# Kernel optimization log

Measured on AMD Instinct MI355X. Metric: run time of the kernel, lower is better.

Reference implementation:

```python
import jax, jax.numpy as jnp
import numpy as np
import math

B, S, HID = 2, 2048, 2048
NH, NKV, HD = 16, 4, 128
N_REP = NH // NKV
THETA = 1000000.0


def apply_rope(x, position_ids, theta=THETA):
    # x: (B, H, S, D), position_ids: (B, S)
    d = x.shape[-1]
    freqs = 1.0 / (theta ** (jnp.arange(0, d, 2, dtype=jnp.float32) / d))  # (D/2,)
    angles = position_ids.astype(jnp.float32)[:, :, None] * freqs[None, None, :]  # (B,S,D/2)
    cos = jnp.cos(angles)[:, None, :, :]  # (B,1,S,D/2)
    sin = jnp.sin(angles)[:, None, :, :]
    x_even = x[..., 0::2]
    x_odd = x[..., 1::2]
    rot_even = x_even * cos - x_odd * sin
    rot_odd = x_even * sin + x_odd * cos
    out = jnp.stack([rot_even, rot_odd], axis=-1)  # (B,H,S,D/2,2)
    return out.reshape(x.shape)


def setup_inputs() -> dict:
    key = jax.random.key(0)
    ks = jax.random.split(key, 6)
    x = jax.random.normal(ks[0], (B, S, HID), dtype=jnp.float32)
    position_ids = jnp.broadcast_to(jnp.arange(S, dtype=jnp.int64)[None, :], (B, S))
    # causal additive mask: 0 on/below diagonal, large negative above
    causal = jnp.where(jnp.tril(jnp.ones((S, S), dtype=bool)), 0.0, -1e9).astype(jnp.float32)
    attention_mask = jnp.broadcast_to(causal[None, None, :, :], (B, 1, S, S))
    sc = 1.0 / math.sqrt(HID)
    Wq = jax.random.normal(ks[1], (HID, NH * HD), dtype=jnp.float32) * sc
    Wk = jax.random.normal(ks[2], (HID, NKV * HD), dtype=jnp.float32) * sc
    Wv = jax.random.normal(ks[3], (HID, NKV * HD), dtype=jnp.float32) * sc
    Wo = jax.random.normal(ks[4], (NH * HD, HID), dtype=jnp.float32) * sc
    return {"x": x, "position_ids": position_ids, "attention_mask": attention_mask,
            "Wq": Wq, "Wk": Wk, "Wv": Wv, "Wo": Wo}


def reference(x, position_ids, attention_mask, Wq, Wk, Wv, Wo):
    b, s, _ = x.shape
    q = (x @ Wq).reshape(b, s, NH, HD).transpose(0, 2, 1, 3)   # (B,NH,S,D)
    k = (x @ Wk).reshape(b, s, NKV, HD).transpose(0, 2, 1, 3)  # (B,NKV,S,D)
    v = (x @ Wv).reshape(b, s, NKV, HD).transpose(0, 2, 1, 3)
    q = apply_rope(q, position_ids)
    k = apply_rope(k, position_ids)
    # repeat_kv: expand KV heads to match Q heads
    k = jnp.repeat(k, N_REP, axis=1)  # (B,NH,S,D)
    v = jnp.repeat(v, N_REP, axis=1)
    scale = 1.0 / math.sqrt(HD)
    scores = jnp.einsum('bhqd,bhkd->bhqk', q, k) * scale
    scores = scores + attention_mask
    attn = jax.nn.softmax(scores, axis=-1)
    out = jnp.einsum('bhqk,bhkd->bhqd', attn, v)
    out = out.transpose(0, 2, 1, 3).reshape(b, s, NH * HD)
    return out @ Wo
```

## Files before the change

### kernel.cpp

```cpp
#include <hip/hip_runtime.h>
#include <hip/hip_bf16.h>

#define S_LEN 2048
#define HID_D 2048
#define NH 16
#define NKV 4
#define HD 128
#define BATCH 2

typedef __hip_bfloat16 bf16;
using f32x4 = __attribute__((ext_vector_type(4))) float;
using s16x8 = __attribute__((ext_vector_type(8))) short;

__device__ __forceinline__ f32x4 mfma_16x16x32(s16x8 a, s16x8 b, f32x4 c) {
  return __builtin_amdgcn_mfma_f32_16x16x32_bf16(a, b, c, 0, 0, 0);
}

__device__ __forceinline__ void gload16(const void* g, void* l) {
  __builtin_amdgcn_global_load_lds(
      (const __attribute__((address_space(1))) void*)g,
      (__attribute__((address_space(3))) void*)l, 16, 0, 0);
}

__device__ __forceinline__ unsigned int pk2bf(float a, float b) {
  __hip_bfloat16 lo = __float2bfloat16(a), hi = __float2bfloat16(b);
  return ((unsigned int)*(unsigned short*)&hi << 16) | *(unsigned short*)&lo;
}

__global__ __launch_bounds__(256) void convert_bf16_k(const float* __restrict__ in,
                                                      bf16* __restrict__ out) {
  int i = (blockIdx.x * 256 + threadIdx.x) * 4;
  float4 v = *(const float4*)&in[i];
  out[i + 0] = __float2bfloat16(v.x);
  out[i + 1] = __float2bfloat16(v.y);
  out[i + 2] = __float2bfloat16(v.z);
  out[i + 3] = __float2bfloat16(v.w);
}

__global__ __launch_bounds__(256) void transpose_convert_k(const float* __restrict__ in,
                                                           bf16* __restrict__ out,
                                                           int K, int N) {
  __shared__ float tile[32][33];
  int n0 = blockIdx.x * 32, k0 = blockIdx.y * 32;
  int tx = threadIdx.x, ty = threadIdx.y;
#pragma unroll
  for (int i = ty; i < 32; i += 8) tile[i][tx] = in[(size_t)(k0 + i) * N + n0 + tx];
  __syncthreads();
#pragma unroll
  for (int i = ty; i < 32; i += 8)
    out[(size_t)(n0 + i) * K + k0 + tx] = __float2bfloat16(tile[tx][i]);
}

__global__ __launch_bounds__(512) void gemm256_k(const bf16* __restrict__ A,
                                                 const bf16* __restrict__ Bt,
                                                 bf16* __restrict__ C,
                                                 int M, int N, int K) {
  __shared__ bf16 Asm[2][256 * 64];
  __shared__ bf16 Bsm[2][256 * 64];
  const int tid = threadIdx.x;
  const int lane = tid & 63, wid = tid >> 6;
  const int fr = lane & 15, hi = lane >> 4;

  const int bid = blockIdx.y * gridDim.x + blockIdx.x;
  const int nwg = gridDim.x * gridDim.y;
  const int swz = (bid & 7) * (nwg >> 3) + (bid >> 3);
  const int m0 = (swz % gridDim.x) * 256;
  const int n0 = (swz / gridDim.x) * 256;

  const bf16* Ag = A + (size_t)m0 * K;
  const bf16* Bg = Bt + (size_t)n0 * K;

  auto stageT = [&](const bf16* src, bf16* ldsBase, int k0) {
#pragma unroll
    for (int c = 0; c < 4; ++c) {
      int byte = tid * 16 + c * 8192;
      int row = byte >> 7;
      int col = byte & 127;
      int colSw = col ^ ((row & 7) << 4);
      gload16((const char*)(src + (size_t)row * K + k0) + colSw,
              (char*)ldsBase + byte);
    }
  };

  f32x4 acc[4][8];
#pragma unroll
  for (int m = 0; m < 4; ++m)
#pragma unroll
    for (int n = 0; n < 8; ++n) acc[m][n] = (f32x4){0.f, 0.f, 0.f, 0.f};

  const int r0 = (wid >> 1) * 64;
  const int c0 = (wid & 1) * 128;
  const int NT = K >> 6;

  stageT(Ag, &Asm[0][0], 0);
  stageT(Bg, &Bsm[0][0], 0);
  asm volatile("s_waitcnt vmcnt(0)" ::: "memory");
  __builtin_amdgcn_s_barrier();

  for (int t = 0; t < NT; ++t) {
    const int cur = t & 1;
    const int nxt = cur ^ 1;
    const int kn = (t + 1) << 6;
    const bool more = (t + 1) < NT;
#pragma unroll
    for (int p = 0; p < 2; ++p) {
      s16x8 af[4], bq[8];
#pragma unroll
      for (int m = 0; m < 4; ++m) {
        int r = r0 + m * 16 + fr;
        int cb = (p * 64 + hi * 16) ^ ((r & 7) << 4);
        af[m] = *(const s16x8*)((const char*)&Asm[cur][0] + r * 128 + cb);
      }
#pragma unroll
      for (int n = 0; n < 8; ++n) {
        int bn = c0 + n * 16 + fr;
        int cb = (p * 64 + hi * 16) ^ ((bn & 7) << 4);
        bq[n] = *(const s16x8*)((const char*)&Bsm[cur][0] + bn * 128 + cb);
      }
      if (p == 0) {
        if (more) {
          stageT(Ag, &Asm[nxt][0], kn);
          stageT(Bg, &Bsm[nxt][0], kn);
        }
      } else {
        asm volatile("s_waitcnt vmcnt(0)" ::: "memory");
      }
      __builtin_amdgcn_s_barrier();

      __builtin_amdgcn_s_setprio(1);
#pragma unroll
      for (int m = 0; m < 4; ++m)
#pragma unroll
        for (int n = 0; n < 8; ++n)
          acc[m][n] = mfma_16x16x32(af[m], bq[n], acc[m][n]);
      __builtin_amdgcn_s_setprio(0);
    }
  }

#pragma unroll
  for (int m = 0; m < 4; ++m)
#pragma unroll
    for (int n = 0; n < 8; ++n) {
      const int row = m0 + r0 + m * 16 + hi * 4;
      const int col = n0 + c0 + n * 16 + fr;
#pragma unroll
      for (int r = 0; r < 4; ++r)
        C[(size_t)(row + r) * N + col] = __float2bfloat16(acc[m][n][r]);
    }
}

__global__ __launch_bounds__(256) void gemm128sq_k(const bf16* __restrict__ A,
                                                   const bf16* __restrict__ Bt,
                                                   float* __restrict__ C,
                                                   int M, int N, int K) {
  __shared__ bf16 Asm[2][128 * 64];
  __shared__ bf16 Bsm[2][128 * 64];
  const int tid = threadIdx.x;
  const int lane = tid & 63, wid = tid >> 6;
  const int fr = lane & 15, hi = lane >> 4;

  const int bid = blockIdx.y * gridDim.x + blockIdx.x;
  const int nwg = gridDim.x * gridDim.y;
  const int swz = (bid & 7) * (nwg >> 3) + (bid >> 3);
  const int m0 = (swz % gridDim.x) * 128;
  const int n0 = (swz / gridDim.x) * 128;

  const bf16* Ag = A + (size_t)m0 * K;
  const bf16* Bg = Bt + (size_t)n0 * K;

  auto stageT = [&](const bf16* src, bf16* ldsBase, int k0) {
#pragma unroll
    for (int c = 0; c < 4; ++c) {
      int byte = tid * 16 + c * 4096;
      int row = byte >> 7;
      int col = byte & 127;
      int colSw = col ^ ((row & 7) << 4);
      gload16((const char*)(src + (size_t)row * K + k0) + colSw,
              (char*)ldsBase + byte);
    }
  };

  f32x4 acc[4][4];
#pragma unroll
  for (int m = 0; m < 4; ++m)
#pragma unroll
    for (int n = 0; n < 4; ++n) acc[m][n] = (f32x4){0.f, 0.f, 0.f, 0.f};

  const int r0 = (wid >> 1) * 64;
  const int c0 = (wid & 1) * 64;
  const int NT = K >> 6;

  stageT(Ag, &Asm[0][0], 0);
  stageT(Bg, &Bsm[0][0], 0);
  asm volatile("s_waitcnt vmcnt(0)" ::: "memory");
  __builtin_amdgcn_s_barrier();

  for (int t = 0; t < NT; ++t) {
    const int cur = t & 1;
    const int nxt = cur ^ 1;
    const int kn = (t + 1) << 6;
    const bool more = (t + 1) < NT;
#pragma unroll
    for (int p = 0; p < 2; ++p) {
      s16x8 af[4], bq[4];
#pragma unroll
      for (int m = 0; m < 4; ++m) {
        int r = r0 + m * 16 + fr;
        int cb = (p * 64 + hi * 16) ^ ((r & 7) << 4);
        af[m] = *(const s16x8*)((const char*)&Asm[cur][0] + r * 128 + cb);
      }
#pragma unroll
      for (int n = 0; n < 4; ++n) {
        int bn = c0 + n * 16 + fr;
        int cb = (p * 64 + hi * 16) ^ ((bn & 7) << 4);
        bq[n] = *(const s16x8*)((const char*)&Bsm[cur][0] + bn * 128 + cb);
      }
      if (p == 0) {
        if (more) {
          stageT(Ag, &Asm[nxt][0], kn);
          stageT(Bg, &Bsm[nxt][0], kn);
        }
      } else {
        asm volatile("s_waitcnt vmcnt(0)" ::: "memory");
      }
      __builtin_amdgcn_s_barrier();

      __builtin_amdgcn_s_setprio(1);
#pragma unroll
      for (int m = 0; m < 4; ++m)
#pragma unroll
        for (int n = 0; n < 4; ++n)
          acc[m][n] = mfma_16x16x32(af[m], bq[n], acc[m][n]);
      __builtin_amdgcn_s_setprio(0);
    }
  }

#pragma unroll
  for (int m = 0; m < 4; ++m)
#pragma unroll
    for (int n = 0; n < 4; ++n) {
      const int row = m0 + r0 + m * 16 + hi * 4;
      const int col = n0 + c0 + n * 16 + fr;
#pragma unroll
      for (int r = 0; r < 4; ++r)
        C[(size_t)(row + r) * N + col] = acc[m][n][r];
    }
}

__global__ __launch_bounds__(256) void rope_q_k(const bf16* __restrict__ qkv,
                                                const int* __restrict__ pos_ids,
                                                bf16* __restrict__ Q) {
  int idx = blockIdx.x * 256 + threadIdx.x;
  int i = idx & 63;
  int h = (idx >> 6) & 15;
  int s = (idx >> 10) & 2047;
  int b = idx >> 21;
  const float kscale = 0.12751841418861862f;
  float pos = (float)pos_ids[b * S_LEN + s];
  float freq = exp2f((float)i * -0.31143075889569023f);
  float ang = pos * freq;
  float sn, cs;
  sincosf(ang, &sn, &cs);
  const bf16* src = qkv + (size_t)(b * S_LEN + s) * 3072 + h * HD + 2 * i;
  float e = __bfloat162float(src[0]), o = __bfloat162float(src[1]);
  bf16* dst = Q + ((size_t)(b * NH + h) * S_LEN + s) * HD + 2 * i;
  dst[0] = __float2bfloat16((e * cs - o * sn) * kscale);
  dst[1] = __float2bfloat16((e * sn + o * cs) * kscale);
}

__global__ __launch_bounds__(256) void rope_k_k(const bf16* __restrict__ qkv,
                                                const int* __restrict__ pos_ids,
                                                bf16* __restrict__ Kd) {
  int idx = blockIdx.x * 256 + threadIdx.x;
  int i = idx & 63;
  int kvh = (idx >> 6) & 3;
  int s = (idx >> 8) & 2047;
  int b = idx >> 19;
  float pos = (float)pos_ids[b * S_LEN + s];
  float freq = exp2f((float)i * -0.31143075889569023f);
  float ang = pos * freq;
  float sn, cs;
  sincosf(ang, &sn, &cs);
  const bf16* src = qkv + (size_t)(b * S_LEN + s) * 3072 + 2048 + kvh * HD + 2 * i;
  float e = __bfloat162float(src[0]), o = __bfloat162float(src[1]);
  bf16* dst = Kd + ((size_t)(b * NKV + kvh) * S_LEN + s) * HD + 2 * i;
  dst[0] = __float2bfloat16(e * cs - o * sn);
  dst[1] = __float2bfloat16(e * sn + o * cs);
}

__global__ __launch_bounds__(256) void v_trans_k(const bf16* __restrict__ qkv,
                                                 bf16* __restrict__ Vt) {
  __shared__ unsigned short tile[32][33];
  const int tx = threadIdx.x, ty = threadIdx.y;
  const int s0 = blockIdx.x * 32;
  const int d0 = blockIdx.y * 32;
  const int b = blockIdx.z >> 2, kvh = blockIdx.z & 3;
  const unsigned short* src = (const unsigned short*)qkv + 2560 + kvh * HD;
#pragma unroll
  for (int i = ty; i < 32; i += 8)
    tile[i][tx] = src[(size_t)(b * S_LEN + s0 + i) * 3072 + d0 + tx];
  __syncthreads();
  unsigned short* dst = (unsigned short*)Vt + (size_t)(b * NKV + kvh) * HD * S_LEN;
#pragma unroll
  for (int i = ty; i < 32; i += 8)
    dst[(size_t)(d0 + i) * S_LEN + s0 + tx] = tile[tx][i];
}

__global__ __launch_bounds__(512) void attn_k(const bf16* __restrict__ Q,
                                              const bf16* __restrict__ K,
                                              const bf16* __restrict__ Vt,
                                              bf16* __restrict__ Aout) {
  __shared__ __align__(16) char KsB[2][8320];
  __shared__ __align__(16) char VsB[2][10240];
  __shared__ __align__(16) char PsB[8][2560];

  const int tid = threadIdx.x;
  const int lane = tid & 63, wid = tid >> 6;
  const int fr = lane & 15, hi = lane >> 4;
  const int pi = blockIdx.x, h = blockIdx.y, b = blockIdx.z;
  const int kvh = h >> 2;
  const bf16* Qh = Q + (size_t)(b * NH + h) * S_LEN * HD;
  const bf16* Kh = K + (size_t)(b * NKV + kvh) * S_LEN * HD;
  const bf16* Vh = Vt + (size_t)(b * NKV + kvh) * HD * S_LEN;

  const int qb = (wid < 4) ? pi : (15 - pi);
  const int q0w = qb * 128 + (wid & 3) * 32;
  const int nsteps = 4 * (15 - pi) + 4;

  s16x8 qf[2][4];
#pragma unroll
  for (int u = 0; u < 2; ++u)
#pragma unroll
    for (int ks = 0; ks < 4; ++ks)
      qf[u][ks] = *(const s16x8*)&Qh[(size_t)(q0w + u * 16 + fr) * HD + ks * 32 + hi * 8];

  f32x4 o[2][8];
#pragma unroll
  for (int u = 0; u < 2; ++u)
#pragma unroll
    for (int ds = 0; ds < 8; ++ds) o[u][ds] = (f32x4){0.f, 0.f, 0.f, 0.f};
  float lacc[2][4];
#pragma unroll
  for (int u = 0; u < 2; ++u)
#pragma unroll
    for (int r = 0; r < 4; ++r) lacc[u][r] = 0.f;

  auto stageK = [&](int bufi, int kv0) {
    gload16((const char*)Kh + ((size_t)(kv0 + wid * 4)) * 256 + lane * 16,
            &KsB[bufi][0] + wid * 1040);
  };
  const int vd = tid >> 2;
  const int vko = (tid & 3) * 8;
  auto vload = [&](int kv0) {
    return *(const s16x8*)&Vh[(size_t)vd * S_LEN + kv0 + vko];
  };

  stageK(0, 0);
  {
    s16x8 v0 = vload(0);
    *(s16x8*)(&VsB[0][0] + vd * 80 + (tid & 3) * 16) = v0;
  }
  __syncthreads();

  int buf = 0;
  for (int s = 0; s < nsteps; ++s) {
    const int kv0 = s * 32;
    const bool more = (s + 1) < nsteps;
    s16x8 vnext = {};
    if (more) {
      stageK(buf ^ 1, kv0 + 32);
      vnext = vload(kv0 + 32);
    }

    if (kv0 <= q0w) {
      const bool diag = (kv0 == q0w);
      f32x4 sg[2][2];
#pragma unroll
      for (int u = 0; u < 2; ++u)
#pragma unroll
        for (int kv = 0; kv < 2; ++kv) sg[u][kv] = (f32x4){0.f, 0.f, 0.f, 0.f};
#pragma unroll
      for (int kv = 0; kv < 2; ++kv) {
        const int row = 2 * fr + kv;
        const char* kbase = &KsB[buf][0] + (row >> 2) * 1040 + (row & 3) * 256;
#pragma unroll
        for (int ks = 0; ks < 4; ++ks) {
          s16x8 kf = *(const s16x8*)(kbase + ks * 64 + hi * 16);
          sg[0][kv] = mfma_16x16x32(qf[0][ks], kf, sg[0][kv]);
          sg[1][kv] = mfma_16x16x32(qf[1][ks], kf, sg[1][kv]);
        }
      }

#pragma unroll
      for (int u = 0; u < 2; ++u)
#pragma unroll
        for (int r = 0; r < 4; ++r) {
          float p0 = __builtin_exp2f(sg[u][0][r]);
          float p1 = __builtin_exp2f(sg[u][1][r]);
          if (diag) {
            const int qrow = u * 16 + hi * 4 + r;
            p0 = (2 * fr <= qrow) ? p0 : 0.f;
            p1 = (2 * fr + 1 <= qrow) ? p1 : 0.f;
          }
          lacc[u][r] += p0 + p1;
          const int prow = u * 16 + hi * 4 + r;
          *(unsigned int*)(&PsB[wid][0] + prow * 80 + fr * 4) = pk2bf(p0, p1);
        }
      __builtin_amdgcn_wave_barrier();

      s16x8 pf[2];
#pragma unroll
      for (int u = 0; u < 2; ++u)
        pf[u] = *(const s16x8*)(&PsB[wid][0] + (u * 16 + fr) * 80 + hi * 16);
      __builtin_amdgcn_wave_barrier();

#pragma unroll
      for (int ds = 0; ds < 8; ++ds) {
        s16x8 vf = *(const s16x8*)(&VsB[buf][0] + (ds * 16 + fr) * 80 + hi * 16);
        o[0][ds] = mfma_16x16x32(pf[0], vf, o[0][ds]);
        o[1][ds] = mfma_16x16x32(pf[1], vf, o[1][ds]);
      }
    }

    if (more)
      *(s16x8*)(&VsB[buf ^ 1][0] + vd * 80 + (tid & 3) * 16) = vnext;
    __syncthreads();
    buf ^= 1;
  }

#pragma unroll
  for (int u = 0; u < 2; ++u)
#pragma unroll
    for (int r = 0; r < 4; ++r) {
      float l = lacc[u][r];
      l += __shfl_xor(l, 1, 16);
      l += __shfl_xor(l, 2, 16);
      l += __shfl_xor(l, 4, 16);
      l += __shfl_xor(l, 8, 16);
      float inv = 1.0f / l;
      const int srow = q0w + u * 16 + hi * 4 + r;
      bf16* orow = Aout + ((size_t)b * S_LEN + srow) * HID_D + h * HD;
#pragma unroll
      for (int ds = 0; ds < 8; ++ds)
        orow[ds * 16 + fr] = __float2bfloat16(o[u][ds][r] * inv);
    }
}

extern "C" void kernel_launch(void* const* d_in, const int* in_sizes, int n_in,
                              void* d_out, int out_size, void* d_ws, size_t ws_size,
                              hipStream_t stream) {
  const float* x = (const float*)d_in[0];
  const int* pos = (const int*)d_in[1];
  const float* Wq = (const float*)d_in[3];
  const float* Wk = (const float*)d_in[4];
  const float* Wv = (const float*)d_in[5];
  const float* Wo = (const float*)d_in[6];
  float* out = (float*)d_out;

  char* ws = (char*)d_ws;
  size_t off = 0;
  auto alloc = [&](size_t bytes) {
    char* p = ws + off;
    off += (bytes + 255) & ~(size_t)255;
    return p;
  };
  bf16* xb = (bf16*)alloc((size_t)4096 * 2048 * 2);
  bf16* WqkvT = (bf16*)alloc((size_t)3072 * 2048 * 2);
  bf16* WoT = (bf16*)alloc((size_t)2048 * 2048 * 2);
  bf16* qkv = (bf16*)alloc((size_t)4096 * 3072 * 2);
  bf16* Qb = (bf16*)alloc((size_t)BATCH * NH * S_LEN * HD * 2);
  bf16* Kb = (bf16*)alloc((size_t)BATCH * NKV * S_LEN * HD * 2);
  bf16* Vtb = (bf16*)alloc((size_t)BATCH * NKV * HD * S_LEN * 2);
  bf16* aout = (bf16*)qkv;

  convert_bf16_k<<<8192, 256, 0, stream>>>(x, xb);
  dim3 tb(32, 8);
  transpose_convert_k<<<dim3(64, 64), tb, 0, stream>>>(Wq, WqkvT, 2048, 2048);
  transpose_convert_k<<<dim3(16, 64), tb, 0, stream>>>(Wk, WqkvT + (size_t)2048 * 2048, 2048, 512);
  transpose_convert_k<<<dim3(16, 64), tb, 0, stream>>>(Wv, WqkvT + (size_t)2560 * 2048, 2048, 512);
  transpose_convert_k<<<dim3(64, 64), tb, 0, stream>>>(Wo, WoT, 2048, 2048);

  gemm256_k<<<dim3(16, 12), 512, 0, stream>>>(xb, WqkvT, qkv, 4096, 3072, 2048);

  rope_q_k<<<16384, 256, 0, stream>>>(qkv, pos, Qb);
  rope_k_k<<<4096, 256, 0, stream>>>(qkv, pos, Kb);
  v_trans_k<<<dim3(64, 4, 8), tb, 0, stream>>>(qkv, Vtb);

  attn_k<<<dim3(8, NH, BATCH), 512, 0, stream>>>(Qb, Kb, Vtb, aout);

  gemm128sq_k<<<dim3(32, 16), 256, 0, stream>>>(aout, WoT, out, 4096, 2048, 2048);
}
```

Before: 233.9 us.

## Split attention into one q-block per workgroup with swizzled async K/V staging

Removes the paired-q-block load balancing (8 waves covering blocks pi and 15-pi). Each 256-thread workgroup now handles a single 128-row q block, launched heaviest-first, over a 16-wide grid. K and V tiles are both staged with direct global-to-LDS loads using an XOR swizzle instead of padding, and the register round-trip for V is dropped. This gives more, smaller workgroups and less LDS per block, at the cost of uneven per-block work that relies on the reversed launch order for balance.

```diff
diff --git a/kernel.cpp b/kernel.cpp
--- a/kernel.cpp
+++ b/kernel.cpp
@@ -306,26 +306,48 @@
     dst[(size_t)(d0 + i) * S_LEN + s0 + tx] = tile[tx][i];
 }
 
-__global__ __launch_bounds__(512) void attn_k(const bf16* __restrict__ Q,
+__global__ __launch_bounds__(256) void attn_k(const bf16* __restrict__ Q,
                                               const bf16* __restrict__ K,
                                               const bf16* __restrict__ Vt,
                                               bf16* __restrict__ Aout) {
-  __shared__ __align__(16) char KsB[2][8320];
-  __shared__ __align__(16) char VsB[2][10240];
-  __shared__ __align__(16) char PsB[8][2560];
+  __shared__ __align__(16) char KsB[2][8192];
+  __shared__ __align__(16) char VsB[2][8192];
+  __shared__ __align__(16) char PsB[4][2560];
 
   const int tid = threadIdx.x;
   const int lane = tid & 63, wid = tid >> 6;
   const int fr = lane & 15, hi = lane >> 4;
-  const int pi = blockIdx.x, h = blockIdx.y, b = blockIdx.z;
+  const int qb = 15 - blockIdx.x;
+  const int h = blockIdx.y, b = blockIdx.z;
   const int kvh = h >> 2;
   const bf16* Qh = Q + (size_t)(b * NH + h) * S_LEN * HD;
   const bf16* Kh = K + (size_t)(b * NKV + kvh) * S_LEN * HD;
   const bf16* Vh = Vt + (size_t)(b * NKV + kvh) * HD * S_LEN;
 
-  const int qb = (wid < 4) ? pi : (15 - pi);
-  const int q0w = qb * 128 + (wid & 3) * 32;
-  const int nsteps = 4 * (15 - pi) + 4;
+  const int q0w = qb * 128 + wid * 32;
+  const int nsteps = 4 * qb + 4;
+
+  auto stageK = [&](int bufi, int kv0) {
+#pragma unroll
+    for (int c = 0; c < 2; ++c) {
+      int X = tid * 16 + c * 4096;
+      int row = X >> 8, col = X & 255;
+      int colSw = col ^ (((row >> 1) & 7) << 4);
+      gload16((const char*)Kh + (size_t)(kv0 + row) * 256 + colSw,
+              &KsB[bufi][0] + X);
+    }
+  };
+  auto stageV = [&](int bufi, int kv0) {
+#pragma unroll
+    for (int c = 0; c < 2; ++c) {
+      int X = tid * 16 + c * 4096;
+      int line = X >> 7, off = X & 127;
+      int offS = off ^ ((line & 7) << 4);
+      int d = 2 * line + (offS >> 6);
+      gload16((const char*)Vh + (size_t)d * (S_LEN * 2) + (size_t)kv0 * 2 + (offS & 63),
+              &VsB[bufi][0] + X);
+    }
+  };
 
   s16x8 qf[2][4];
 #pragma unroll
@@ -345,31 +367,16 @@
 #pragma unroll
     for (int r = 0; r < 4; ++r) lacc[u][r] = 0.f;
 
-  auto stageK = [&](int bufi, int kv0) {
-    gload16((const char*)Kh + ((size_t)(kv0 + wid * 4)) * 256 + lane * 16,
-            &KsB[bufi][0] + wid * 1040);
-  };
-  const int vd = tid >> 2;
-  const int vko = (tid & 3) * 8;
-  auto vload = [&](int kv0) {
-    return *(const s16x8*)&Vh[(size_t)vd * S_LEN + kv0 + vko];
-  };
-
   stageK(0, 0);
-  {
-    s16x8 v0 = vload(0);
-    *(s16x8*)(&VsB[0][0] + vd * 80 + (tid & 3) * 16) = v0;
-  }
+  stageV(0, 0);
   __syncthreads();
 
   int buf = 0;
   for (int s = 0; s < nsteps; ++s) {
     const int kv0 = s * 32;
-    const bool more = (s + 1) < nsteps;
-    s16x8 vnext = {};
-    if (more) {
+    if (s + 1 < nsteps) {
       stageK(buf ^ 1, kv0 + 32);
-      vnext = vload(kv0 + 32);
+      stageV(buf ^ 1, kv0 + 32);
     }
 
     if (kv0 <= q0w) {
@@ -378,16 +385,17 @@
 #pragma unroll
       for (int u = 0; u < 2; ++u)
 #pragma unroll
-        for (int kv = 0; kv < 2; ++kv) sg[u][kv] = (f32x4){0.f, 0.f, 0.f, 0.f};
-#pragma unroll
-      for (int kv = 0; kv < 2; ++kv) {
-        const int row = 2 * fr + kv;
-        const char* kbase = &KsB[buf][0] + (row >> 2) * 1040 + (row & 3) * 256;
+        for (int kvi = 0; kvi < 2; ++kvi) sg[u][kvi] = (f32x4){0.f, 0.f, 0.f, 0.f};
+#pragma unroll
+      for (int kvi = 0; kvi < 2; ++kvi) {
+        const int row = 2 * fr + kvi;
+        const char* kb_ = &KsB[buf][0] + row * 256;
+        const int sw = ((row >> 1) & 7) << 4;
 #pragma unroll
         for (int ks = 0; ks < 4; ++ks) {
-          s16x8 kf = *(const s16x8*)(kbase + ks * 64 + hi * 16);
-          sg[0][kv] = mfma_16x16x32(qf[0][ks], kf, sg[0][kv]);
-          sg[1][kv] = mfma_16x16x32(qf[1][ks], kf, sg[1][kv]);
+          s16x8 kf = *(const s16x8*)(kb_ + ((ks * 64 + hi * 16) ^ sw));
+          sg[0][kvi] = mfma_16x16x32(qf[0][ks], kf, sg[0][kvi]);
+          sg[1][kvi] = mfma_16x16x32(qf[1][ks], kf, sg[1][kvi]);
         }
       }
 
@@ -398,9 +406,9 @@
           float p0 = __builtin_exp2f(sg[u][0][r]);
           float p1 = __builtin_exp2f(sg[u][1][r]);
           if (diag) {
-            const int qrow = u * 16 + hi * 4 + r;
-            p0 = (2 * fr <= qrow) ? p0 : 0.f;
-            p1 = (2 * fr + 1 <= qrow) ? p1 : 0.f;
+            const int rowrel = u * 16 + hi * 4 + r;
+            p0 = (2 * fr <= rowrel) ? p0 : 0.f;
+            p1 = (2 * fr + 1 <= rowrel) ? p1 : 0.f;
           }
           lacc[u][r] += p0 + p1;
           const int prow = u * 16 + hi * 4 + r;
@@ -416,14 +424,15 @@
 
 #pragma unroll
       for (int ds = 0; ds < 8; ++ds) {
-        s16x8 vf = *(const s16x8*)(&VsB[buf][0] + (ds * 16 + fr) * 80 + hi * 16);
+        const int d = ds * 16 + fr;
+        const int line = d >> 1;
+        const int off = ((d & 1) * 64 + hi * 16) ^ ((line & 7) << 4);
+        s16x8 vf = *(const s16x8*)(&VsB[buf][0] + line * 128 + off);
         o[0][ds] = mfma_16x16x32(pf[0], vf, o[0][ds]);
         o[1][ds] = mfma_16x16x32(pf[1], vf, o[1][ds]);
       }
     }
 
-    if (more)
-      *(s16x8*)(&VsB[buf ^ 1][0] + vd * 80 + (tid & 3) * 16) = vnext;
     __syncthreads();
     buf ^= 1;
   }
@@ -486,7 +495,7 @@
   rope_k_k<<<4096, 256, 0, stream>>>(qkv, pos, Kb);
   v_trans_k<<<dim3(64, 4, 8), tb, 0, stream>>>(qkv, Vtb);
 
-  attn_k<<<dim3(8, NH, BATCH), 512, 0, stream>>>(Qb, Kb, Vtb, aout);
+  attn_k<<<dim3(16, NH, BATCH), 256, 0, stream>>>(Qb, Kb, Vtb, aout);
 
   gemm128sq_k<<<dim3(32, 16), 256, 0, stream>>>(aout, WoT, out, 4096, 2048, 2048);
 }
```

After: 256.8 us. 9.8% more time.
